# Kernel optimization log

Hardware: AMD Instinct MI355X
Metric: run time of the kernel (lower is better)

Reference implementation:

```python
import jax, jax.numpy as jnp
import numpy as np

B, T, V = 16, 512, 8000
BLANK = 0
LSM = 0.1
W_SOFT = 0.5


def setup_inputs() -> dict:
    rng = np.random.default_rng(0)
    key = jax.random.key(0)
    k1, k2 = jax.random.split(key)

    align = rng.integers(1, V, size=(B, T))
    align = np.where(rng.random((B, T)) < 0.6, BLANK, align)
    align[:, 0] = rng.integers(1, V, size=B)  # guarantee >=1 non-blank run
    xlens = rng.integers(T // 2, T + 1, size=B)
    frame_mask = np.arange(T)[None, :] < xlens[:, None]
    align = np.where(frame_mask, align, BLANK)  # zero out padding frames

    # derive consistent ylens = number of non-blank runs within xlen
    nonblank = align != BLANK
    shifted = np.concatenate([np.full((B, 1), BLANK, dtype=align.dtype), align[:, :-1]], axis=1)
    ylens = (nonblank & (align != shifted)).sum(axis=1)

    ys = rng.integers(1, V, size=(B, T))  # hard labels, L = T (safe upper bound)
    logits = jax.random.normal(k1, (B, T, V), dtype=jnp.float32)
    soft_labels = jax.nn.softmax(jax.random.normal(k2, (B, T, V), dtype=jnp.float32), axis=-1)

    return {
        "logits": logits,
        "ys": jnp.asarray(ys, dtype=jnp.int32),
        "soft_labels": soft_labels,
        "aligns": jnp.asarray(align, dtype=jnp.int32),
        "xlens": jnp.asarray(xlens, dtype=jnp.int32),
        "ylens": jnp.asarray(ylens, dtype=jnp.int32),
    }


def reference(logits, ys, soft_labels, aligns, xlens, ylens):
    # position='all': every non-blank frame t maps to its run index (label_id).
    frame_mask = jnp.arange(T)[None, :] < xlens[:, None]          # [B,T]
    a = jnp.where(frame_mask, aligns, BLANK)
    nonblank = a != BLANK                                          # = label_exists
    shifted = jnp.pad(a[:, :-1], ((0, 0), (1, 0)), constant_values=BLANK)
    run_start = nonblank & (a != shifted)
    label_id = jnp.cumsum(run_start.astype(jnp.int32), axis=1) - 1  # [B,T]
    lm = jnp.maximum(label_id, 0)                                  # clamp; masked where blank

    logp = jax.nn.log_softmax(logits, axis=-1)                     # [B,T,V]
    n_exists = nonblank.sum(axis=1).astype(logp.dtype)             # [B]

    # soft part: sum_v soft_labels[b, lm[b,t], v] * logp[b,t,v]
    soft_g = jnp.take_along_axis(soft_labels, lm[:, :, None], axis=1)  # [B,T,V]
    frame_soft = jnp.sum(soft_g * logp, axis=-1)                   # [B,T]
    loss_soft = jnp.sum(jnp.where(nonblank, frame_soft, 0.0), axis=1) / n_exists

    # hard part with label smoothing: (1-e)*logp[y] + e/(V-1)*(sum_v logp - logp[y])
    y_t = jnp.take_along_axis(ys, lm, axis=1)                      # [B,T]
    logp_y = jnp.take_along_axis(logp, y_t[:, :, None], axis=2)[..., 0]
    sum_lp = jnp.sum(logp, axis=-1)
    frame_hard = (1.0 - LSM) * logp_y + (LSM / (V - 1)) * (sum_lp - logp_y)
    loss_hard = jnp.sum(jnp.where(nonblank, frame_hard, 0.0), axis=1) / n_exists

    per_b = W_SOFT * loss_soft + (1.0 - W_SOFT) * loss_hard
    return -jnp.mean(per_b)
```

## Files before the change

kernel.cpp:

```cpp
#include <hip/hip_runtime.h>
#include <math.h>

#define BB 16
#define TT 512
#define VV 8000
#define BLANK 0
#define LSM 0.1f
#define W_SOFT 0.5f
#define BLOCK 256

__global__ __launch_bounds__(TT) void meta_kernel(
    const int* __restrict__ aligns,
    const int* __restrict__ xlens,
    int* __restrict__ meta,
    float* __restrict__ inv_nexists,
    float* __restrict__ out) {
  int b = blockIdx.x;
  int t = threadIdx.x;
  if (b == 0 && t == 0) out[0] = 0.0f;

  int xlen = xlens[b];
  int a  = (t < xlen) ? aligns[b * TT + t] : BLANK;
  int ap = BLANK;
  if (t > 0) ap = ((t - 1) < xlen) ? aligns[b * TT + t - 1] : BLANK;
  int nonblank = (a != BLANK) ? 1 : 0;
  int runstart = (nonblank && (a != ap)) ? 1 : 0;

  int lane = t & 63;
  int w = t >> 6;

  int val = runstart;
#pragma unroll
  for (int off = 1; off < 64; off <<= 1) {
    int v = __shfl_up(val, off);
    if (lane >= off) val += v;
  }
  int cnt = nonblank;
#pragma unroll
  for (int off = 32; off > 0; off >>= 1) cnt += __shfl_xor(cnt, off);

  __shared__ int wsum[8], wcnt[8];
  if (lane == 63) wsum[w] = val;
  if (lane == 0)  wcnt[w] = cnt;
  __syncthreads();

  int base = 0;
#pragma unroll
  for (int i = 0; i < 8; ++i) if (i < w) base += wsum[i];
  meta[b * TT + t] = nonblank ? (base + val - 1) : -1;

  if (t == 0) {
    int total = 0;
#pragma unroll
    for (int i = 0; i < 8; ++i) total += wcnt[i];
    inv_nexists[b] = 1.0f / (float)total;
  }
}

__global__ __launch_bounds__(BLOCK) void frame_kernel(
    const float* __restrict__ logits,
    const int* __restrict__ ys,
    const float* __restrict__ soft,
    const int* __restrict__ meta,
    const float* __restrict__ inv_nexists,
    float* __restrict__ out) {
  int idx = blockIdx.x;
  int lm = meta[idx];
  if (lm < 0) return;
  int b = idx >> 9;

  __shared__ float red[8];

  const float* xrow = logits + (size_t)idx * VV;
  const float* srow = soft + ((size_t)(b * TT + lm)) * VV;
  int tid = threadIdx.x;
  int wid = tid >> 6;

  float4 xr[8], sr[8];
#pragma unroll
  for (int k = 0; k < 8; ++k) {
    int i = tid * 4 + k * (BLOCK * 4);
    if (i < VV) {
      xr[k] = *(const float4*)(xrow + i);
      sr[k] = *(const float4*)(srow + i);
    } else {
      xr[k] = make_float4(-INFINITY, -INFINITY, -INFINITY, -INFINITY);
      sr[k] = make_float4(0.0f, 0.0f, 0.0f, 0.0f);
    }
  }
  int y = ys[b * TT + lm];
  float xy = xrow[y];
  __builtin_amdgcn_sched_barrier(0);

  float tmax = -INFINITY, tsum = 0.0f;
#pragma unroll
  for (int k = 0; k < 8; ++k) {
    int i = tid * 4 + k * (BLOCK * 4);
    if (i < VV) {
      float4 x = xr[k];
      tmax = fmaxf(tmax, fmaxf(fmaxf(x.x, x.y), fmaxf(x.z, x.w)));
      tsum += (x.x + x.y) + (x.z + x.w);
    }
  }
  for (int off = 32; off > 0; off >>= 1) {
    tmax = fmaxf(tmax, __shfl_xor(tmax, off));
    tsum += __shfl_xor(tsum, off);
  }
  if ((tid & 63) == 0) { red[wid] = tmax; red[4 + wid] = tsum; }
  __syncthreads();
  float bmax = fmaxf(fmaxf(red[0], red[1]), fmaxf(red[2], red[3]));
  float bsum = (red[4] + red[5]) + (red[6] + red[7]);
  __syncthreads();

  float tse = 0.0f;
#pragma unroll
  for (int k = 0; k < 8; ++k) {
    tse += __expf(xr[k].x - bmax) + __expf(xr[k].y - bmax) +
           __expf(xr[k].z - bmax) + __expf(xr[k].w - bmax);
  }
  for (int off = 32; off > 0; off >>= 1) tse += __shfl_xor(tse, off);
  if ((tid & 63) == 0) red[wid] = tse;
  __syncthreads();
  float sumexp = (red[0] + red[1]) + (red[2] + red[3]);
  float C = bmax + logf(sumexp);
  __syncthreads();

  float tdot = 0.0f;
#pragma unroll
  for (int k = 0; k < 8; ++k) {
    int i = tid * 4 + k * (BLOCK * 4);
    if (i < VV) {
      float4 sv = sr[k];
      float4 x = xr[k];
      tdot += sv.x * (x.x - C) + sv.y * (x.y - C) +
              sv.z * (x.z - C) + sv.w * (x.w - C);
    }
  }
  for (int off = 32; off > 0; off >>= 1) tdot += __shfl_xor(tdot, off);
  if ((tid & 63) == 0) red[wid] = tdot;
  __syncthreads();

  if (tid == 0) {
    float dot = (red[0] + red[1]) + (red[2] + red[3]);
    float logp_y = xy - C;
    float sum_lp = bsum - (float)VV * C;
    float frame_hard = (1.0f - LSM) * logp_y +
                       (LSM / (float)(VV - 1)) * (sum_lp - logp_y);
    float val = W_SOFT * dot + (1.0f - W_SOFT) * frame_hard;
    atomicAdd(out, -val * inv_nexists[b] * (1.0f / (float)BB));
  }
}

extern "C" void kernel_launch(void* const* d_in, const int* in_sizes, int n_in,
                              void* d_out, int out_size, void* d_ws, size_t ws_size,
                              hipStream_t stream) {
  const float* logits = (const float*)d_in[0];
  const int*   ys     = (const int*)d_in[1];
  const float* soft   = (const float*)d_in[2];
  const int*   aligns = (const int*)d_in[3];
  const int*   xlens  = (const int*)d_in[4];

  int*   meta  = (int*)d_ws;
  float* inv_n = (float*)((char*)d_ws + (size_t)BB * TT * sizeof(int));
  float* out   = (float*)d_out;

  meta_kernel<<<BB, TT, 0, stream>>>(aligns, xlens, meta, inv_n, out);
  frame_kernel<<<BB * TT, BLOCK, 0, stream>>>(logits, ys, soft, meta, inv_n, out);
}
```

Baseline: 432.2 us.

## Fuse run-index scan into frame kernel, recomputing label index per block

Removes the separate metadata kernel and workspace. Each frame block now counts run starts up to its own frame and the total non-blank frames of its batch row with a block-wide reduction. The output is zeroed with a memset instead. This saves a launch and the dependency between the two kernels, at the cost of redundant scan work and an extra barrier in every block, and the soft-label row load now waits on that reduction.

```diff
diff --git a/kernel.cpp b/kernel.cpp
--- a/kernel.cpp
+++ b/kernel.cpp
@@ -9,82 +9,67 @@
 #define W_SOFT 0.5f
 #define BLOCK 256
 
-__global__ __launch_bounds__(TT) void meta_kernel(
-    const int* __restrict__ aligns,
-    const int* __restrict__ xlens,
-    int* __restrict__ meta,
-    float* __restrict__ inv_nexists,
-    float* __restrict__ out) {
-  int b = blockIdx.x;
-  int t = threadIdx.x;
-  if (b == 0 && t == 0) out[0] = 0.0f;
-
-  int xlen = xlens[b];
-  int a  = (t < xlen) ? aligns[b * TT + t] : BLANK;
-  int ap = BLANK;
-  if (t > 0) ap = ((t - 1) < xlen) ? aligns[b * TT + t - 1] : BLANK;
-  int nonblank = (a != BLANK) ? 1 : 0;
-  int runstart = (nonblank && (a != ap)) ? 1 : 0;
-
-  int lane = t & 63;
-  int w = t >> 6;
-
-  int val = runstart;
-#pragma unroll
-  for (int off = 1; off < 64; off <<= 1) {
-    int v = __shfl_up(val, off);
-    if (lane >= off) val += v;
-  }
-  int cnt = nonblank;
-#pragma unroll
-  for (int off = 32; off > 0; off >>= 1) cnt += __shfl_xor(cnt, off);
-
-  __shared__ int wsum[8], wcnt[8];
-  if (lane == 63) wsum[w] = val;
-  if (lane == 0)  wcnt[w] = cnt;
-  __syncthreads();
-
-  int base = 0;
-#pragma unroll
-  for (int i = 0; i < 8; ++i) if (i < w) base += wsum[i];
-  meta[b * TT + t] = nonblank ? (base + val - 1) : -1;
-
-  if (t == 0) {
-    int total = 0;
-#pragma unroll
-    for (int i = 0; i < 8; ++i) total += wcnt[i];
-    inv_nexists[b] = 1.0f / (float)total;
-  }
-}
-
-__global__ __launch_bounds__(BLOCK) void frame_kernel(
+__global__ __launch_bounds__(BLOCK) void fused_kernel(
     const float* __restrict__ logits,
     const int* __restrict__ ys,
     const float* __restrict__ soft,
-    const int* __restrict__ meta,
-    const float* __restrict__ inv_nexists,
+    const int* __restrict__ aligns,
+    const int* __restrict__ xlens,
     float* __restrict__ out) {
   int idx = blockIdx.x;
-  int lm = meta[idx];
-  if (lm < 0) return;
   int b = idx >> 9;
+  int t = idx & (TT - 1);
 
-  __shared__ float red[8];
+  int xlen = xlens[b];
+  if (t >= xlen) return;
+  if (aligns[b * TT + t] == BLANK) return;
+
+  int tid = threadIdx.x;
+  int lane = tid & 63;
+  int wid = tid >> 6;
 
   const float* xrow = logits + (size_t)idx * VV;
-  const float* srow = soft + ((size_t)(b * TT + lm)) * VV;
-  int tid = threadIdx.x;
-  int wid = tid >> 6;
-
-  float4 xr[8], sr[8];
+  float4 xr[8];
 #pragma unroll
   for (int k = 0; k < 8; ++k) {
     int i = tid * 4 + k * (BLOCK * 4);
     if (i < VV) {
       xr[k] = *(const float4*)(xrow + i);
+    } else {
+      xr[k] = make_float4(-INFINITY, -INFINITY, -INFINITY, -INFINITY);
+    }
+  }
+
+  int j0 = tid * 2, j1 = tid * 2 + 1;
+  int a0  = (j0 < xlen) ? aligns[b * TT + j0] : BLANK;
+  int a1  = (j1 < xlen) ? aligns[b * TT + j1] : BLANK;
+  int am1 = (j0 > 0 && (j0 - 1) < xlen) ? aligns[b * TT + j0 - 1] : BLANK;
+
+  int rs0 = (a0 != BLANK && a0 != am1 && j0 <= t) ? 1 : 0;
+  int rs1 = (a1 != BLANK && a1 != a0  && j1 <= t) ? 1 : 0;
+  int nb  = (a0 != BLANK ? 1 : 0) + (a1 != BLANK ? 1 : 0);
+
+  int pack = ((rs0 + rs1) << 16) | nb;
+#pragma unroll
+  for (int off = 32; off > 0; off >>= 1) pack += __shfl_xor(pack, off);
+
+  __shared__ int redi[4];
+  __shared__ float red[8];
+  if (lane == 0) redi[wid] = pack;
+  __syncthreads();
+  int tot = (redi[0] + redi[1]) + (redi[2] + redi[3]);
+  int lm = (tot >> 16) - 1;
+  float inv_n = 1.0f / (float)(tot & 0xffff);
+  __syncthreads();
+
+  const float* srow = soft + ((size_t)(b * TT + lm)) * VV;
+  float4 sr[8];
+#pragma unroll
+  for (int k = 0; k < 8; ++k) {
+    int i = tid * 4 + k * (BLOCK * 4);
+    if (i < VV) {
       sr[k] = *(const float4*)(srow + i);
     } else {
-      xr[k] = make_float4(-INFINITY, -INFINITY, -INFINITY, -INFINITY);
       sr[k] = make_float4(0.0f, 0.0f, 0.0f, 0.0f);
     }
   }
@@ -106,7 +91,7 @@
     tmax = fmaxf(tmax, __shfl_xor(tmax, off));
     tsum += __shfl_xor(tsum, off);
   }
-  if ((tid & 63) == 0) { red[wid] = tmax; red[4 + wid] = tsum; }
+  if (lane == 0) { red[wid] = tmax; red[4 + wid] = tsum; }
   __syncthreads();
   float bmax = fmaxf(fmaxf(red[0], red[1]), fmaxf(red[2], red[3]));
   float bsum = (red[4] + red[5]) + (red[6] + red[7]);
@@ -119,7 +104,7 @@
            __expf(xr[k].z - bmax) + __expf(xr[k].w - bmax);
   }
   for (int off = 32; off > 0; off >>= 1) tse += __shfl_xor(tse, off);
-  if ((tid & 63) == 0) red[wid] = tse;
+  if (lane == 0) red[wid] = tse;
   __syncthreads();
   float sumexp = (red[0] + red[1]) + (red[2] + red[3]);
   float C = bmax + logf(sumexp);
@@ -137,7 +122,7 @@
     }
   }
   for (int off = 32; off > 0; off >>= 1) tdot += __shfl_xor(tdot, off);
-  if ((tid & 63) == 0) red[wid] = tdot;
+  if (lane == 0) red[wid] = tdot;
   __syncthreads();
 
   if (tid == 0) {
@@ -147,7 +132,7 @@
     float frame_hard = (1.0f - LSM) * logp_y +
                        (LSM / (float)(VV - 1)) * (sum_lp - logp_y);
     float val = W_SOFT * dot + (1.0f - W_SOFT) * frame_hard;
-    atomicAdd(out, -val * inv_nexists[b] * (1.0f / (float)BB));
+    atomicAdd(out, -val * inv_n * (1.0f / (float)BB));
   }
 }
 
@@ -160,10 +145,7 @@
   const int*   aligns = (const int*)d_in[3];
   const int*   xlens  = (const int*)d_in[4];
 
-  int*   meta  = (int*)d_ws;
-  float* inv_n = (float*)((char*)d_ws + (size_t)BB * TT * sizeof(int));
-  float* out   = (float*)d_out;
-
-  meta_kernel<<<BB, TT, 0, stream>>>(aligns, xlens, meta, inv_n, out);
-  frame_kernel<<<BB * TT, BLOCK, 0, stream>>>(logits, ys, soft, meta, inv_n, out);
+  float* out = (float*)d_out;
+  hipMemsetAsync(out, 0, sizeof(float), stream);
+  fused_kernel<<<BB * TT, BLOCK, 0, stream>>>(logits, ys, soft, aligns, xlens, out);
 }
```

New measurement: 431.3 us. No clear change (-0.2%).
